# Kernel optimization log

Measured on AMD Instinct MI355X. Metric: run time of the kernel, lower is better.

## Reference

```python
import jax, jax.numpy as jnp
import numpy as np

EPS = 1e-5


def _tconv(x, W, b):
    # x: [M, Cin, S], W: [Cout, Cin, K] -> [M, Cout, S] (SAME padding)
    y = jax.lax.conv_general_dilated(x, W, window_strides=(1,), padding='SAME',
                                     dimension_numbers=('NCH', 'OIH', 'NCH'))
    return y + b[None, :, None]


def _bn(x, g, b, axes, pshape):
    # batch-statistics normalization (train-mode BN, deterministic)
    m = jnp.mean(x, axes, keepdims=True)
    v = jnp.var(x, axes, keepdims=True)
    return (x - m) * jax.lax.rsqrt(v + EPS) * g.reshape(pshape) + b.reshape(pshape)


def setup_inputs() -> dict:
    key = jax.random.key(0)
    ks = jax.random.split(key, 12)
    B, Cin, N, S = 4, 32, 1024, 32
    Cout, Csp, E, K = 64, 64, 16384, 3
    x = jax.random.normal(ks[0], (B, Cin, N, S), dtype=jnp.float32)
    edge_index = jax.random.randint(ks[1], (2, E), 0, N, dtype=jnp.int64)
    sc = 0.05
    return {
        'x': x,
        'edge_index': edge_index,
        'W1': jax.random.normal(ks[2], (Cout, Cin, K), dtype=jnp.float32) * sc,
        'b1': jnp.zeros((Cout,), jnp.float32),
        'g1': jnp.ones((Cout,), jnp.float32),
        'be1': jnp.zeros((Cout,), jnp.float32),
        'Wg': jax.random.normal(ks[3], (Cout, Csp), dtype=jnp.float32) * sc,
        'bg': jnp.zeros((Csp,), jnp.float32),
        'gs': jnp.ones((Csp,), jnp.float32),
        'bes': jnp.zeros((Csp,), jnp.float32),
        'W2': jax.random.normal(ks[4], (Cout, Csp, K), dtype=jnp.float32) * sc,
        'b2': jnp.zeros((Cout,), jnp.float32),
        'g2': jnp.ones((Cout,), jnp.float32),
        'be2': jnp.zeros((Cout,), jnp.float32),
        'Wres': jax.random.normal(ks[5], (Cout, Cin, 1), dtype=jnp.float32) * sc,
        'bres': jnp.zeros((Cout,), jnp.float32),
    }


def reference(x, edge_index, W1, b1, g1, be1, Wg, bg, gs, bes, W2, b2, g2, be2, Wres, bres):
    B, Cin, N, S = x.shape
    Cout = W1.shape[0]
    Csp = Wg.shape[1]

    # ---- temporal1: [B*N, Cin, S] -> [B*N, Cout, S] ----
    x1 = x.transpose(0, 2, 1, 3).reshape(B * N, Cin, S)
    h = jax.nn.relu(_bn(_tconv(x1, W1, b1), g1, be1, (0, 2), (1, -1, 1)))

    # ---- spatial GCN, all B*S timesteps in one pass ----
    h = h.reshape(B, N, Cout, S).transpose(0, 3, 1, 2)  # [B, S, N, Cout]
    hw = jnp.einsum('bsnc,cd->bsnd', h, Wg)             # [B, S, N, Csp]

    # self-loops + symmetric normalization (PyG GCNConv)
    loops = jnp.arange(N, dtype=edge_index.dtype)
    src = jnp.concatenate([edge_index[0], loops])
    dst = jnp.concatenate([edge_index[1], loops])
    deg = jax.ops.segment_sum(jnp.ones_like(src, dtype=hw.dtype), dst, num_segments=N)
    dinv = jnp.where(deg > 0, jax.lax.rsqrt(deg), 0.0)
    norm = (dinv[src] * dinv[dst])[None, None, :, None]  # [1,1,E+N,1]

    msg = hw[:, :, src, :] * norm                        # [B, S, E+N, Csp]
    agg = jnp.zeros_like(hw).at[:, :, dst, :].add(msg) + bg

    # per-timestep BatchNorm1d over the node dim (loop normalized each [N, Csp] slice)
    s = jax.nn.relu(_bn(agg, gs, bes, (2,), (1, 1, 1, -1)))  # dropout: eval mode

    # ---- temporal2: [B*N, Csp, S] -> [B*N, Cout, S] ----
    s = s.transpose(0, 2, 3, 1).reshape(B * N, Csp, S)   # [B,S,N,C] -> [B,N,C,S]
    h2 = jax.nn.relu(_bn(_tconv(s, W2, b2), g2, be2, (0, 2), (1, -1, 1)))
    h2 = h2.reshape(B, N, Cout, S)

    # ---- residual 1x1 conv ----
    res = _tconv(x1, Wres, bres).reshape(B, N, Cout, S)

    out = jax.nn.relu(h2 + res).transpose(0, 2, 1, 3)    # [B, Cout, N, S]
    return out
```

## Files before the change

kernel.cpp:

```cpp
#include <hip/hip_runtime.h>
#include <stdint.h>

#define B_    4
#define CIN   32
#define NN    1024
#define SS    32
#define COUT  64
#define CSP   64
#define EPSV  1e-5f

typedef __attribute__((ext_vector_type(8))) short bfrag;
typedef __attribute__((ext_vector_type(4))) float facc;

__device__ __forceinline__ uint32_t f2b_rne(float f) {
    uint32_t x = __float_as_uint(f);
    return (x + 0x7fffu + ((x >> 16) & 1u)) >> 16;
}
__device__ __forceinline__ float bfu(uint32_t v) { return __uint_as_float(v << 16); }
__device__ __forceinline__ float bfh(uint32_t v) { return __uint_as_float(v & 0xffff0000u); }

__global__ void pack_zero_kernel(const float* __restrict__ W1,
                                 const float* __restrict__ W2,
                                 const float* __restrict__ Wg,
                                 uint32_t* __restrict__ wpk1H, uint32_t* __restrict__ wpk1L,
                                 uint32_t* __restrict__ wpkH, uint32_t* __restrict__ wpkL,
                                 uint32_t* __restrict__ wgpH, uint32_t* __restrict__ wgpL,
                                 int* __restrict__ deg, int* __restrict__ cursor) {
    int blk = blockIdx.x, t = threadIdx.x;
    if (blk < 6) {
        int flat = blk * 256 + t;
        int lane = flat & 63, fi = flat >> 6;
        int kh = fi & 1, q = fi >> 1;
        int tap = q % 3, cc = q / 3;
        int ct = cc & 1, cb2 = cc >> 1;
        int cout = cb2 * 32 + ct * 16 + (lane & 15);
        int cbase = kh * 32 + (lane >> 4) * 8;
        const float* wp = W2 + ((size_t)cout * 64 + cbase) * 3 + tap;
        uint32_t h[8], l[8];
#pragma unroll
        for (int j = 0; j < 8; j++) {
            float w = wp[3 * j];
            uint32_t hb = f2b_rne(w);
            uint32_t lb = f2b_rne(w - bfu(hb));
            h[j] = hb; l[j] = lb;
        }
        uint4 H = {h[0] | (h[1] << 16), h[2] | (h[3] << 16),
                   h[4] | (h[5] << 16), h[6] | (h[7] << 16)};
        uint4 L = {l[0] | (l[1] << 16), l[2] | (l[3] << 16),
                   l[4] | (l[5] << 16), l[6] | (l[7] << 16)};
        ((uint4*)wpkH)[flat] = H;
        ((uint4*)wpkL)[flat] = L;
    } else if (blk < 9) {
        int flat = (blk - 6) * 256 + t;
        int lane = flat & 63, fi = flat >> 6;
        int tap = fi % 3, cc = fi / 3;
        int ct = cc & 1, cb2 = cc >> 1;
        int cout = cb2 * 32 + ct * 16 + (lane & 15);
        int k0 = (lane >> 4) * 8;
        const float* wp = W1 + (size_t)cout * 96 + k0 * 3 + tap;
        uint32_t h[8], l[8];
#pragma unroll
        for (int j = 0; j < 8; j++) {
            float w = wp[3 * j];
            uint32_t hb = f2b_rne(w);
            uint32_t lb = f2b_rne(w - bfu(hb));
            h[j] = hb; l[j] = lb;
        }
        uint4 H = {h[0] | (h[1] << 16), h[2] | (h[3] << 16),
                   h[4] | (h[5] << 16), h[6] | (h[7] << 16)};
        uint4 L = {l[0] | (l[1] << 16), l[2] | (l[3] << 16),
                   l[4] | (l[5] << 16), l[6] | (l[7] << 16)};
        ((uint4*)wpk1H)[flat] = H;
        ((uint4*)wpk1L)[flat] = L;
    } else if (blk < 11) {
        int flat = (blk - 9) * 256 + t;
        int lane = flat & 63, fi = flat >> 6;
        int kh = fi & 1, dt = fi >> 1;
        int d = dt * 16 + (lane & 15);
        int c0 = kh * 32 + (lane >> 4) * 8;
        const float* wp = Wg + (size_t)c0 * CSP + d;
        uint32_t h[8], l[8];
#pragma unroll
        for (int j = 0; j < 8; j++) {
            float w = wp[(size_t)j * CSP];
            uint32_t hb = f2b_rne(w);
            uint32_t lb = f2b_rne(w - bfu(hb));
            h[j] = hb; l[j] = lb;
        }
        uint4 H = {h[0] | (h[1] << 16), h[2] | (h[3] << 16),
                   h[4] | (h[5] << 16), h[6] | (h[7] << 16)};
        uint4 L = {l[0] | (l[1] << 16), l[2] | (l[3] << 16),
                   l[4] | (l[5] << 16), l[6] | (l[7] << 16)};
        ((uint4*)wgpH)[flat] = H;
        ((uint4*)wgpL)[flat] = L;
    } else {
        int4 z = {0, 0, 0, 0};
        ((int4*)deg)[t] = z;
        ((int4*)cursor)[t] = z;
    }
}

__global__ void deg_count_kernel(const int* __restrict__ ei, int E,
                                 int* __restrict__ deg) {
    __shared__ int snz;
    int t = threadIdx.x;
    if (t == 0) snz = 0;
    __syncthreads();
    if (t < 128 && ei[2 * t + 1] != 0) atomicOr(&snz, 1);
    __syncthreads();
    int i64 = (snz == 0) ? 1 : 0;
    int e = blockIdx.x * 256 + t;
    if (e < E) {
        int d = i64 ? ei[2 * (E + e)] : ei[E + e];
        atomicAdd(&deg[d], 1);
    }
}

__global__ __launch_bounds__(1024) void scan_kernel(
    const int* __restrict__ deg, int* __restrict__ row_ptr, float* __restrict__ dinv) {
    __shared__ int sb[NN];
    int t = threadIdx.x;
    int v = deg[t];
    sb[t] = v;
    __syncthreads();
    for (int off = 1; off < NN; off <<= 1) {
        int tmp = (t >= off) ? sb[t - off] : 0;
        __syncthreads();
        sb[t] += tmp;
        __syncthreads();
    }
    row_ptr[t] = sb[t] - v;
    if (t == NN - 1) row_ptr[NN] = sb[t];
    dinv[t] = rsqrtf((float)(v + 1));
}

__global__ void csr_fill_kernel(const int* __restrict__ ei, int E,
                                const int* __restrict__ row_ptr, int* __restrict__ cursor,
                                const float* __restrict__ dinv, int2* __restrict__ edata) {
    __shared__ int snz;
    int t = threadIdx.x;
    if (t == 0) snz = 0;
    __syncthreads();
    if (t < 128 && ei[2 * t + 1] != 0) atomicOr(&snz, 1);
    __syncthreads();
    int i64 = (snz == 0) ? 1 : 0;
    int e = blockIdx.x * 256 + t;
    if (e < E) {
        int s = i64 ? ei[2 * e] : ei[e];
        int d = i64 ? ei[2 * (E + e)] : ei[E + e];
        int pos = atomicAdd(&cursor[d], 1);
        edata[row_ptr[d] + pos] = make_int2(s, __float_as_int(dinv[s]));
    }
}

__global__ __launch_bounds__(256, 2) void conv1_mfma_kernel(
    const float* __restrict__ x, const uint32_t* __restrict__ wpk1H,
    const uint32_t* __restrict__ wpk1L, const float* __restrict__ b1,
    float* __restrict__ h_pre, float* __restrict__ psumC, float* __restrict__ pssC) {
    __shared__ __align__(16) char pool[18432];
    char* Phi = pool;
    char* Plo = pool + 8704;
    float* redS = (float*)(pool + 17408);
    float* redQ = (float*)(pool + 17920);
    int t = threadIdx.x;
    int grp = blockIdx.x;
    int b = grp >> 8, n0 = (grp & 255) * 4;
    int lane = t & 63, wv = t >> 6;
    int s0 = (wv >> 1) * 16, cb = (wv & 1) * 32;
    int l15 = lane & 15, lg = lane >> 4;

    if (t < 32) {
        int nl = t >> 3, rem = t & 7;
        int row = (rem >> 2) ? 33 : 0;
        int q = rem & 3;
        uint32_t off = (uint32_t)(nl * 2176 + row * 64 + q * 16);
        off ^= (uint32_t)((row & 7) << 4);
        *(uint4*)(Phi + off) = make_uint4(0u, 0u, 0u, 0u);
        *(uint4*)(Plo + off) = make_uint4(0u, 0u, 0u, 0u);
    }
#pragma unroll
    for (int it = 0; it < 2; it++) {
        int flat = it * 256 + t;
        int cinp = flat & 15;
        int nl = (flat >> 4) & 3;
        int s4 = (flat >> 6) * 4;
        const float* xp = x + (((size_t)b * CIN + 2 * cinp) * NN + n0 + nl) * SS + s4;
        float4 u0 = *(const float4*)xp;
        float4 u1 = *(const float4*)(xp + NN * SS);
        float va[4] = {u0.x, u0.y, u0.z, u0.w};
        float vb[4] = {u1.x, u1.y, u1.z, u1.w};
#pragma unroll
        for (int j = 0; j < 4; j++) {
            uint32_t ha = f2b_rne(va[j]), hb = f2b_rne(vb[j]);
            uint32_t la = f2b_rne(va[j] - bfu(ha)), lb = f2b_rne(vb[j] - bfu(hb));
            int row = s4 + j + 1;
            uint32_t off = (uint32_t)(nl * 2176 + row * 64 + cinp * 4);
            off ^= (uint32_t)((row & 7) << 4);
            *(uint32_t*)(Phi + off) = ha | (hb << 16);
            *(uint32_t*)(Plo + off) = la | (lb << 16);
        }
    }
    bfrag Wh[2][3], Wl[2][3];
    {
        const uint4* WH = (const uint4*)wpk1H;
        const uint4* WL = (const uint4*)wpk1L;
        int cb2 = wv & 1;
#pragma unroll
        for (int ct = 0; ct < 2; ct++)
#pragma unroll
            for (int tap = 0; tap < 3; tap++) {
                int fi = ((cb2 * 2 + ct) * 3 + tap) * 64 + lane;
                uint4 H = WH[fi];
                uint4 L = WL[fi];
                Wh[ct][tap] = *(const bfrag*)&H;
                Wl[ct][tap] = *(const bfrag*)&L;
            }
    }
    __syncthreads();

    float bb0 = b1[cb + l15], bb1 = b1[cb + 16 + l15];
    float sS0 = 0.f, sS1 = 0.f, sQ0 = 0.f, sQ1 = 0.f;
    for (int nl = 0; nl < 4; nl++) {
        facc acc0 = {0.f, 0.f, 0.f, 0.f};
        facc acc1 = {0.f, 0.f, 0.f, 0.f};
#pragma unroll
        for (int tap = 0; tap < 3; tap++) {
            int row = s0 + tap + l15;
            uint32_t off = (uint32_t)(nl * 2176 + row * 64 + (lg << 4));
            off ^= (uint32_t)((row & 7) << 4);
            bfrag ah = *(const bfrag*)(Phi + off);
            bfrag al = *(const bfrag*)(Plo + off);
            acc0 = __builtin_amdgcn_mfma_f32_16x16x32_bf16(ah, Wh[0][tap], acc0, 0, 0, 0);
            acc1 = __builtin_amdgcn_mfma_f32_16x16x32_bf16(ah, Wh[1][tap], acc1, 0, 0, 0);
            acc0 = __builtin_amdgcn_mfma_f32_16x16x32_bf16(al, Wh[0][tap], acc0, 0, 0, 0);
            acc1 = __builtin_amdgcn_mfma_f32_16x16x32_bf16(al, Wh[1][tap], acc1, 0, 0, 0);
            acc0 = __builtin_amdgcn_mfma_f32_16x16x32_bf16(ah, Wl[0][tap], acc0, 0, 0, 0);
            acc1 = __builtin_amdgcn_mfma_f32_16x16x32_bf16(ah, Wl[1][tap], acc1, 0, 0, 0);
        }
        int sx = s0 + (lg << 2);
        float* hp = h_pre + ((size_t)(b * NN + n0 + nl)) * (COUT * SS);
        {
            float y0 = acc0[0] + bb0, y1 = acc0[1] + bb0;
            float y2 = acc0[2] + bb0, y3 = acc0[3] + bb0;
            float4 o = {y0, y1, y2, y3};
            *(float4*)(hp + (cb + l15) * SS + sx) = o;
            sS0 += y0 + y1 + y2 + y3;
            sQ0 += y0 * y0 + y1 * y1 + y2 * y2 + y3 * y3;
        }
        {
            float y0 = acc1[0] + bb1, y1 = acc1[1] + bb1;
            float y2 = acc1[2] + bb1, y3 = acc1[3] + bb1;
            float4 o = {y0, y1, y2, y3};
            *(float4*)(hp + (cb + 16 + l15) * SS + sx) = o;
            sS1 += y0 + y1 + y2 + y3;
            sQ1 += y0 * y0 + y1 * y1 + y2 * y2 + y3 * y3;
        }
    }
    sS0 += __shfl_down(sS0, 16); sS0 += __shfl_down(sS0, 32);
    sS1 += __shfl_down(sS1, 16); sS1 += __shfl_down(sS1, 32);
    sQ0 += __shfl_down(sQ0, 16); sQ0 += __shfl_down(sQ0, 32);
    sQ1 += __shfl_down(sQ1, 16); sQ1 += __shfl_down(sQ1, 32);
    if (lane < 16) {
        redS[wv * 32 + lane] = sS0;      redQ[wv * 32 + lane] = sQ0;
        redS[wv * 32 + 16 + lane] = sS1; redQ[wv * 32 + 16 + lane] = sQ1;
    }
    __syncthreads();
    if (t < 64) {
        int wA = t >> 5, slot = t & 31;
        float S = redS[wA * 32 + slot] + redS[(wA + 2) * 32 + slot];
        float Q = redQ[wA * 32 + slot] + redQ[(wA + 2) * 32 + slot];
        psumC[(size_t)t * 1024 + grp] = S;
        pssC[(size_t)t * 1024 + grp] = Q;
    }
}

__global__ void bn_reduce_kernel(const float* __restrict__ psum, const float* __restrict__ pss,
                                 const float* __restrict__ g, const float* __restrict__ be,
                                 float* __restrict__ scale, float* __restrict__ shift,
                                 float invM, int stride, int nslots) {
    int c = blockIdx.x, t = threadIdx.x;
    const float* ps = psum + c * stride;
    const float* pq = pss + c * stride;
    float s = 0.f, q = 0.f;
    for (int i = t; i < nslots; i += 256) { s += ps[i]; q += pq[i]; }
#pragma unroll
    for (int o = 32; o > 0; o >>= 1) { s += __shfl_down(s, o); q += __shfl_down(q, o); }
    __shared__ float ws_[4], wq_[4];
    if ((t & 63) == 0) { ws_[t >> 6] = s; wq_[t >> 6] = q; }
    __syncthreads();
    if (t == 0) {
        float S = ws_[0] + ws_[1] + ws_[2] + ws_[3];
        float Q = wq_[0] + wq_[1] + wq_[2] + wq_[3];
        float m = S * invM, v = Q * invM - m * m;
        float sc = g[c] * rsqrtf(v + EPSV);
        scale[c] = sc;
        shift[c] = be[c] - m * sc;
    }
}

__global__ __launch_bounds__(256, 2) void bn1_gemm_mfma_kernel(
    const float* __restrict__ h_pre, const float* __restrict__ scale1,
    const float* __restrict__ shift1, const uint32_t* __restrict__ wgpH,
    const uint32_t* __restrict__ wgpL, ushort* __restrict__ hw) {
    __shared__ __align__(16) char pool[32768];
    char* Xhi = pool;
    char* Xlo = pool + 16384;
    int t = threadIdx.x;
    int grp = blockIdx.x;
    int b = grp >> 8, n0 = (grp & 255) * 4;
    int lane = t & 63, wv = t >> 6;
    int l15 = lane & 15, lg = lane >> 4;

#pragma unroll
    for (int it = 0; it < 4; it++) {
        int flat = it * 256 + t;
        int sq = flat & 7;
        int nl = (flat >> 3) & 3;
        int cp = flat >> 5;
        int c = 2 * cp;
        int s4 = sq * 4;
        const float* p = h_pre + (((size_t)(b * NN + n0 + nl)) * COUT + c) * SS + s4;
        float4 u0 = *(const float4*)p;
        float4 u1 = *(const float4*)(p + SS);
        float scA = scale1[c], shA = shift1[c];
        float scB = scale1[c + 1], shB = shift1[c + 1];
        float va[4] = {fmaxf(u0.x * scA + shA, 0.f), fmaxf(u0.y * scA + shA, 0.f),
                       fmaxf(u0.z * scA + shA, 0.f), fmaxf(u0.w * scA + shA, 0.f)};
        float vb[4] = {fmaxf(u1.x * scB + shB, 0.f), fmaxf(u1.y * scB + shB, 0.f),
                       fmaxf(u1.z * scB + shB, 0.f), fmaxf(u1.w * scB + shB, 0.f)};
#pragma unroll
        for (int j = 0; j < 4; j++) {
            uint32_t ha = f2b_rne(va[j]), hb = f2b_rne(vb[j]);
            uint32_t la = f2b_rne(va[j] - bfu(ha)), lb = f2b_rne(vb[j] - bfu(hb));
            int row = nl * 32 + s4 + j;
            uint32_t off = (uint32_t)(row * 128 + 4 * cp);
            off ^= (uint32_t)((row & 7) << 4);
            *(uint32_t*)(Xhi + off) = ha | (hb << 16);
            *(uint32_t*)(Xlo + off) = la | (lb << 16);
        }
    }
    bfrag WgH[4][2], WgL[4][2];
    {
        const uint4* WH = (const uint4*)wgpH;
        const uint4* WL = (const uint4*)wgpL;
#pragma unroll
        for (int dt = 0; dt < 4; dt++)
#pragma unroll
            for (int kh = 0; kh < 2; kh++) {
                int fi = (dt * 2 + kh) * 64 + lane;
                uint4 H = WH[fi];
                uint4 L = WL[fi];
                WgH[dt][kh] = *(const bfrag*)&H;
                WgL[dt][kh] = *(const bfrag*)&L;
            }
    }
    __syncthreads();

    int n = n0 + wv;
#pragma unroll
    for (int rt = 0; rt < 2; rt++) {
        facc a0 = {0.f, 0.f, 0.f, 0.f};
        facc a1 = {0.f, 0.f, 0.f, 0.f};
        facc a2 = {0.f, 0.f, 0.f, 0.f};
        facc a3 = {0.f, 0.f, 0.f, 0.f};
#pragma unroll
        for (int kh = 0; kh < 2; kh++) {
            int row = wv * 32 + rt * 16 + l15;
            uint32_t off = (uint32_t)(row * 128 + kh * 64 + (lg << 4));
            off ^= (uint32_t)((row & 7) << 4);
            bfrag xh = *(const bfrag*)(Xhi + off);
            bfrag xl = *(const bfrag*)(Xlo + off);
            a0 = __builtin_amdgcn_mfma_f32_16x16x32_bf16(WgH[0][kh], xh, a0, 0, 0, 0);
            a1 = __builtin_amdgcn_mfma_f32_16x16x32_bf16(WgH[1][kh], xh, a1, 0, 0, 0);
            a2 = __builtin_amdgcn_mfma_f32_16x16x32_bf16(WgH[2][kh], xh, a2, 0, 0, 0);
            a3 = __builtin_amdgcn_mfma_f32_16x16x32_bf16(WgH[3][kh], xh, a3, 0, 0, 0);
            a0 = __builtin_amdgcn_mfma_f32_16x16x32_bf16(WgL[0][kh], xh, a0, 0, 0, 0);
            a1 = __builtin_amdgcn_mfma_f32_16x16x32_bf16(WgL[1][kh], xh, a1, 0, 0, 0);
            a2 = __builtin_amdgcn_mfma_f32_16x16x32_bf16(WgL[2][kh], xh, a2, 0, 0, 0);
            a3 = __builtin_amdgcn_mfma_f32_16x16x32_bf16(WgL[3][kh], xh, a3, 0, 0, 0);
            a0 = __builtin_amdgcn_mfma_f32_16x16x32_bf16(WgH[0][kh], xl, a0, 0, 0, 0);
            a1 = __builtin_amdgcn_mfma_f32_16x16x32_bf16(WgH[1][kh], xl, a1, 0, 0, 0);
            a2 = __builtin_amdgcn_mfma_f32_16x16x32_bf16(WgH[2][kh], xl, a2, 0, 0, 0);
            a3 = __builtin_amdgcn_mfma_f32_16x16x32_bf16(WgH[3][kh], xl, a3, 0, 0, 0);
        }
        int s = rt * 16 + l15;
        ushort* op = hw + (((size_t)(b * NN + n)) * SS + s) * CSP;
        {
            uint32_t p0 = f2b_rne(a0[0]) | (f2b_rne(a0[1]) << 16);
            uint32_t p1 = f2b_rne(a0[2]) | (f2b_rne(a0[3]) << 16);
            *(uint2*)(op + 0 * 16 + lg * 4) = make_uint2(p0, p1);
        }
        {
            uint32_t p0 = f2b_rne(a1[0]) | (f2b_rne(a1[1]) << 16);
            uint32_t p1 = f2b_rne(a1[2]) | (f2b_rne(a1[3]) << 16);
            *(uint2*)(op + 1 * 16 + lg * 4) = make_uint2(p0, p1);
        }
        {
            uint32_t p0 = f2b_rne(a2[0]) | (f2b_rne(a2[1]) << 16);
            uint32_t p1 = f2b_rne(a2[2]) | (f2b_rne(a2[3]) << 16);
            *(uint2*)(op + 2 * 16 + lg * 4) = make_uint2(p0, p1);
        }
        {
            uint32_t p0 = f2b_rne(a3[0]) | (f2b_rne(a3[1]) << 16);
            uint32_t p1 = f2b_rne(a3[2]) | (f2b_rne(a3[3]) << 16);
            *(uint2*)(op + 3 * 16 + lg * 4) = make_uint2(p0, p1);
        }
    }
}

__global__ __launch_bounds__(256, 4) void gcn_kernel(
    const ushort* __restrict__ hw, const int* __restrict__ row_ptr,
    const int2* __restrict__ edata, const float* __restrict__ dinv,
    const float* __restrict__ bg, float* __restrict__ agg,
    float* __restrict__ psum2, float* __restrict__ pss2) {
    int t = threadIdx.x;
    int blk = blockIdx.x;
    int xcd = blk & 7, jj = blk >> 3;
    int b = xcd >> 1;
    int grp = (xcd & 1) + 2 * jj;
    int n0 = grp * 4;
    int off = t * 8;
    const ushort* hwb = hw + (size_t)b * NN * 2048;
    float bgv[8];
    int c0 = off & 63;
#pragma unroll
    for (int j = 0; j < 8; j++) bgv[j] = bg[c0 + j];
    float sS[8], sQ[8];
#pragma unroll
    for (int j = 0; j < 8; j++) { sS[j] = 0.f; sQ[j] = 0.f; }
    for (int g = 0; g < 4; g++) {
        int n = n0 + g;
        int r0 = row_ptr[n], r1 = row_ptr[n + 1];
        float dn = dinv[n];
        float acc[8];
        {
            uint4 u = *(const uint4*)(hwb + (size_t)n * 2048 + off);
            acc[0] = dn * bfu(u.x); acc[1] = dn * bfh(u.x);
            acc[2] = dn * bfu(u.y); acc[3] = dn * bfh(u.y);
            acc[4] = dn * bfu(u.z); acc[5] = dn * bfh(u.z);
            acc[6] = dn * bfu(u.w); acc[7] = dn * bfh(u.w);
        }
        int r = r0;
        for (; r + 4 <= r1; r += 4) {
            int2 e0 = edata[r], e1 = edata[r + 1];
            int2 e2 = edata[r + 2], e3 = edata[r + 3];
            uint4 u0 = *(const uint4*)(hwb + (size_t)e0.x * 2048 + off);
            uint4 u1 = *(const uint4*)(hwb + (size_t)e1.x * 2048 + off);
            uint4 u2 = *(const uint4*)(hwb + (size_t)e2.x * 2048 + off);
            uint4 u3 = *(const uint4*)(hwb + (size_t)e3.x * 2048 + off);
            float w0 = __int_as_float(e0.y), w1 = __int_as_float(e1.y);
            float w2 = __int_as_float(e2.y), w3 = __int_as_float(e3.y);
            acc[0] += w0 * bfu(u0.x) + w1 * bfu(u1.x);
            acc[1] += w0 * bfh(u0.x) + w1 * bfh(u1.x);
            acc[2] += w0 * bfu(u0.y) + w1 * bfu(u1.y);
            acc[3] += w0 * bfh(u0.y) + w1 * bfh(u1.y);
            acc[4] += w0 * bfu(u0.z) + w1 * bfu(u1.z);
            acc[5] += w0 * bfh(u0.z) + w1 * bfh(u1.z);
            acc[6] += w0 * bfu(u0.w) + w1 * bfu(u1.w);
            acc[7] += w0 * bfh(u0.w) + w1 * bfh(u1.w);
            acc[0] += w2 * bfu(u2.x) + w3 * bfu(u3.x);
            acc[1] += w2 * bfh(u2.x) + w3 * bfh(u3.x);
            acc[2] += w2 * bfu(u2.y) + w3 * bfu(u3.y);
            acc[3] += w2 * bfh(u2.y) + w3 * bfh(u3.y);
            acc[4] += w2 * bfu(u2.z) + w3 * bfu(u3.z);
            acc[5] += w2 * bfh(u2.z) + w3 * bfh(u3.z);
            acc[6] += w2 * bfu(u2.w) + w3 * bfu(u3.w);
            acc[7] += w2 * bfh(u2.w) + w3 * bfh(u3.w);
        }
        for (; r < r1; r++) {
            int2 e = edata[r];
            uint4 u = *(const uint4*)(hwb + (size_t)e.x * 2048 + off);
            float w = __int_as_float(e.y);
            acc[0] += w * bfu(u.x); acc[1] += w * bfh(u.x);
            acc[2] += w * bfu(u.y); acc[3] += w * bfh(u.y);
            acc[4] += w * bfu(u.z); acc[5] += w * bfh(u.z);
            acc[6] += w * bfu(u.w); acc[7] += w * bfh(u.w);
        }
        float o[8];
#pragma unroll
        for (int j = 0; j < 8; j++) {
            o[j] = dn * acc[j] + bgv[j];
            sS[j] += o[j]; sQ[j] += o[j] * o[j];
        }
        float* ar = agg + ((size_t)(b * NN + n)) * 2048 + off;
        float4 o0 = {o[0], o[1], o[2], o[3]}, o1 = {o[4], o[5], o[6], o[7]};
        *(float4*)ar = o0; *(float4*)(ar + 4) = o1;
    }
    float* ps = psum2 + ((size_t)(b * 256 + grp)) * 2048 + off;
    float* pq = pss2 + ((size_t)(b * 256 + grp)) * 2048 + off;
    float4 s0v = {sS[0], sS[1], sS[2], sS[3]}, s1v = {sS[4], sS[5], sS[6], sS[7]};
    float4 q0v = {sQ[0], sQ[1], sQ[2], sQ[3]}, q1v = {sQ[4], sQ[5], sQ[6], sQ[7]};
    *(float4*)ps = s0v; *(float4*)(ps + 4) = s1v;
    *(float4*)pq = q0v; *(float4*)(pq + 4) = q1v;
}

__global__ __launch_bounds__(256) void bn2_reduce_kernel(
    const float* __restrict__ psum2, const float* __restrict__ pss2,
    const float* __restrict__ gs, const float* __restrict__ bes,
    float* __restrict__ scale2, float* __restrict__ shift2) {
    __shared__ float redS[4][32], redQ[4][32];
    int t = threadIdx.x;
    int slot = blockIdx.x * 32 + (t & 31);
    int b = slot >> 11, rem = slot & 2047;
    int chunk = t >> 5;
    const float* ps = psum2 + ((size_t)(b * 256 + chunk * 32)) * 2048 + rem;
    const float* pq = pss2 + ((size_t)(b * 256 + chunk * 32)) * 2048 + rem;
    float S = 0.f, Q = 0.f;
#pragma unroll 8
    for (int i = 0; i < 32; i++) {
        S += ps[(size_t)i * 2048];
        Q += pq[(size_t)i * 2048];
    }
    S += __shfl_down(S, 32);
    Q += __shfl_down(Q, 32);
    int w = t >> 6;
    if ((t & 63) < 32) { redS[w][t & 31] = S; redQ[w][t & 31] = Q; }
    __syncthreads();
    if (t < 32) {
        float Sf = redS[0][t] + redS[1][t] + redS[2][t] + redS[3][t];
        float Qf = redQ[0][t] + redQ[1][t] + redQ[2][t] + redQ[3][t];
        int slot0 = blockIdx.x * 32 + t;
        int d = slot0 & 63;
        float m = Sf * (1.f / NN);
        float v = Qf * (1.f / NN) - m * m;
        float sc = gs[d] * rsqrtf(v + EPSV);
        scale2[slot0] = sc;
        shift2[slot0] = bes[d] - m * sc;
    }
}

__global__ __launch_bounds__(256, 2) void conv2_mfma_kernel(
    const float* __restrict__ agg, const float* __restrict__ scale2,
    const float* __restrict__ shift2, const uint32_t* __restrict__ wpkH,
    const uint32_t* __restrict__ wpkL,
    const float* __restrict__ b2, float* __restrict__ h2_pre,
    float* __restrict__ psumC, float* __restrict__ pssC) {
    __shared__ __align__(16) char pool[35840];
    char* Phi = pool;
    char* Plo = pool + 17408;
    float* redS = (float*)(pool + 34816);
    float* redQ = (float*)(pool + 35328);
    int t = threadIdx.x;
    int grp = blockIdx.x;
    int b = grp >> 8, n0 = (grp & 255) * 4;
    int lane = t & 63, wv = t >> 6;
    int s0 = (wv >> 1) * 16, cb = (wv & 1) * 32;
    int l15 = lane & 15, lg = lane >> 4;

    if (t < 128) {
        int nl = t >> 5, rem = t & 31;
        int tr = (rem >> 4) ? 33 : 0;
        int j = rem & 15;
        uint32_t off = (uint32_t)(nl * 4352 + tr * 128 + 8 * j);
        off ^= (uint32_t)((tr & 7) << 4);
        *(uint2*)(Phi + off) = make_uint2(0u, 0u);
        *(uint2*)(Plo + off) = make_uint2(0u, 0u);
    }
#pragma unroll
    for (int i = 0; i < 8; i++) {
        int flat4 = i * 256 + t;
        int c0 = 4 * (flat4 & 15);
        int s = (flat4 >> 4) & 31;
        int nl = flat4 >> 9;
        const float* p = agg + ((size_t)((b * NN + n0 + nl) * 32 + s)) * 64 + c0;
        float4 u = *(const float4*)p;
        int bsi = (b * 32 + s) * 64 + c0;
        float4 sc = *(const float4*)(scale2 + bsi);
        float4 sh = *(const float4*)(shift2 + bsi);
        float v0 = fmaxf(u.x * sc.x + sh.x, 0.f);
        float v1 = fmaxf(u.y * sc.y + sh.y, 0.f);
        float v2 = fmaxf(u.z * sc.z + sh.z, 0.f);
        float v3 = fmaxf(u.w * sc.w + sh.w, 0.f);
        uint32_t h0 = f2b_rne(v0), h1 = f2b_rne(v1), h2 = f2b_rne(v2), h3 = f2b_rne(v3);
        uint32_t l0 = f2b_rne(v0 - bfu(h0)), l1 = f2b_rne(v1 - bfu(h1));
        uint32_t l2 = f2b_rne(v2 - bfu(h2)), l3 = f2b_rne(v3 - bfu(h3));
        int tr = s + 1;
        uint32_t off = (uint32_t)(nl * 4352 + tr * 128 + 2 * c0);
        off ^= (uint32_t)((tr & 7) << 4);
        *(uint2*)(Phi + off) = make_uint2(h0 | (h1 << 16), h2 | (h3 << 16));
        *(uint2*)(Plo + off) = make_uint2(l0 | (l1 << 16), l2 | (l3 << 16));
    }

    bfrag Wh[2][3][2], Wl[2][3][2];
    {
        const uint4* WH = (const uint4*)wpkH;
        const uint4* WL = (const uint4*)wpkL;
        int cb2 = wv & 1;
#pragma unroll
        for (int ct = 0; ct < 2; ct++)
#pragma unroll
            for (int tap = 0; tap < 3; tap++)
#pragma unroll
                for (int kh = 0; kh < 2; kh++) {
                    int fi = ((((cb2 * 2 + ct) * 3 + tap) * 2) + kh) * 64 + lane;
                    uint4 H = WH[fi];
                    uint4 L = WL[fi];
                    Wh[ct][tap][kh] = *(const bfrag*)&H;
                    Wl[ct][tap][kh] = *(const bfrag*)&L;
                }
    }
    __syncthreads();

    float bb0 = b2[cb + l15], bb1 = b2[cb + 16 + l15];
    float sS0 = 0.f, sS1 = 0.f, sQ0 = 0.f, sQ1 = 0.f;
    for (int nl = 0; nl < 4; nl++) {
        facc acc0 = {0.f, 0.f, 0.f, 0.f};
        facc acc1 = {0.f, 0.f, 0.f, 0.f};
#pragma unroll
        for (int tap = 0; tap < 3; tap++) {
#pragma unroll
            for (int kh = 0; kh < 2; kh++) {
                int row = s0 + tap + l15;
                uint32_t off = (uint32_t)(nl * 4352 + row * 128 + kh * 64 + (lg << 4));
                off ^= (uint32_t)((row & 7) << 4);
                bfrag ah = *(const bfrag*)(Phi + off);
                bfrag al = *(const bfrag*)(Plo + off);
                acc0 = __builtin_amdgcn_mfma_f32_16x16x32_bf16(ah, Wh[0][tap][kh], acc0, 0, 0, 0);
                acc1 = __builtin_amdgcn_mfma_f32_16x16x32_bf16(ah, Wh[1][tap][kh], acc1, 0, 0, 0);
                acc0 = __builtin_amdgcn_mfma_f32_16x16x32_bf16(al, Wh[0][tap][kh], acc0, 0, 0, 0);
                acc1 = __builtin_amdgcn_mfma_f32_16x16x32_bf16(al, Wh[1][tap][kh], acc1, 0, 0, 0);
                acc0 = __builtin_amdgcn_mfma_f32_16x16x32_bf16(ah, Wl[0][tap][kh], acc0, 0, 0, 0);
                acc1 = __builtin_amdgcn_mfma_f32_16x16x32_bf16(ah, Wl[1][tap][kh], acc1, 0, 0, 0);
            }
        }
        int sx = s0 + (lg << 2);
        float* hp = h2_pre + ((size_t)(b * NN + n0 + nl)) * (COUT * SS);
        {
            float y0 = acc0[0] + bb0, y1 = acc0[1] + bb0;
            float y2 = acc0[2] + bb0, y3 = acc0[3] + bb0;
            float4 o = {y0, y1, y2, y3};
            *(float4*)(hp + (cb + l15) * SS + sx) = o;
            sS0 += y0 + y1 + y2 + y3;
            sQ0 += y0 * y0 + y1 * y1 + y2 * y2 + y3 * y3;
        }
        {
            float y0 = acc1[0] + bb1, y1 = acc1[1] + bb1;
            float y2 = acc1[2] + bb1, y3 = acc1[3] + bb1;
            float4 o = {y0, y1, y2, y3};
            *(float4*)(hp + (cb + 16 + l15) * SS + sx) = o;
            sS1 += y0 + y1 + y2 + y3;
            sQ1 += y0 * y0 + y1 * y1 + y2 * y2 + y3 * y3;
        }
    }
    sS0 += __shfl_down(sS0, 16); sS0 += __shfl_down(sS0, 32);
    sS1 += __shfl_down(sS1, 16); sS1 += __shfl_down(sS1, 32);
    sQ0 += __shfl_down(sQ0, 16); sQ0 += __shfl_down(sQ0, 32);
    sQ1 += __shfl_down(sQ1, 16); sQ1 += __shfl_down(sQ1, 32);
    if (lane < 16) {
        redS[wv * 32 + lane] = sS0;      redQ[wv * 32 + lane] = sQ0;
        redS[wv * 32 + 16 + lane] = sS1; redQ[wv * 32 + 16 + lane] = sQ1;
    }
    __syncthreads();
    if (t < 64) {
        int wA = t >> 5, slot = t & 31;
        float S = redS[wA * 32 + slot] + redS[(wA + 2) * 32 + slot];
        float Q = redQ[wA * 32 + slot] + redQ[(wA + 2) * 32 + slot];
        psumC[(size_t)t * 1024 + grp] = S;
        pssC[(size_t)t * 1024 + grp] = Q;
    }
}

__global__ __launch_bounds__(256) void final_kernel(
    const float* __restrict__ x, const float* __restrict__ Wres,
    const float* __restrict__ bres, const float* __restrict__ h2_pre,
    const float* __restrict__ scale3, const float* __restrict__ shift3,
    float* __restrict__ out) {
    __shared__ __align__(16) float xs[CIN][36];
    __shared__ float wrl[COUT * 33];
    int t = threadIdx.x;
    int bn = blockIdx.x;
    int b = bn >> 10, n = bn & (NN - 1);
    {
        int sst = t & 31, cinb = t >> 5;
#pragma unroll
        for (int i = 0; i < 4; i++) {
            int cin = cinb + 8 * i;
            xs[cin][sst] = x[(((size_t)b * CIN + cin) * NN + n) * SS + sst];
        }
    }
#pragma unroll
    for (int i = 0; i < 2; i++) {
        int lin = (i * 256 + t) * 4;
        int cw = lin >> 5, c0 = lin & 31;
        float4 v = *(const float4*)(Wres + lin);
        float* dst = &wrl[cw * 33 + c0];
        dst[0] = v.x; dst[1] = v.y; dst[2] = v.z; dst[3] = v.w;
    }
    __syncthreads();
    int cout = t >> 2, s0 = (t & 3) * 8;
    float res[8];
    float bb = bres[cout];
#pragma unroll
    for (int j = 0; j < 8; j++) res[j] = bb;
    const float* wrow = &wrl[cout * 33];
#pragma unroll 4
    for (int cin = 0; cin < CIN; cin++) {
        float w = wrow[cin];
        float4 xa = *(const float4*)&xs[cin][s0];
        float4 xb = *(const float4*)&xs[cin][s0 + 4];
        res[0] += xa.x * w; res[1] += xa.y * w; res[2] += xa.z * w; res[3] += xa.w * w;
        res[4] += xb.x * w; res[5] += xb.y * w; res[6] += xb.z * w; res[7] += xb.w * w;
    }
    const float* hp = h2_pre + (size_t)bn * COUT * SS + cout * SS + s0;
    float4 h0 = *(const float4*)hp, h1 = *(const float4*)(hp + 4);
    float h2[8] = {h0.x, h0.y, h0.z, h0.w, h1.x, h1.y, h1.z, h1.w};
    float sc = scale3[cout], sh = shift3[cout];
    float o[8];
#pragma unroll
    for (int j = 0; j < 8; j++) {
        float hv = fmaxf(sc * h2[j] + sh, 0.f);
        o[j] = fmaxf(hv + res[j], 0.f);
    }
    float* op = out + (((size_t)b * COUT + cout) * NN + n) * SS + s0;
    float4 o0 = {o[0], o[1], o[2], o[3]}, o1 = {o[4], o[5], o[6], o[7]};
    *(float4*)op = o0; *(float4*)(op + 4) = o1;
}

extern "C" void kernel_launch(void* const* d_in, const int* in_sizes, int n_in,
                              void* d_out, int out_size, void* d_ws, size_t ws_size,
                              hipStream_t stream) {
    const float* x    = (const float*)d_in[0];
    const int*   ei   = (const int*)  d_in[1];
    const float* W1   = (const float*)d_in[2];
    const float* b1   = (const float*)d_in[3];
    const float* g1   = (const float*)d_in[4];
    const float* be1  = (const float*)d_in[5];
    const float* Wg   = (const float*)d_in[6];
    const float* bg   = (const float*)d_in[7];
    const float* gs   = (const float*)d_in[8];
    const float* bes  = (const float*)d_in[9];
    const float* W2   = (const float*)d_in[10];
    const float* b2   = (const float*)d_in[11];
    const float* g2   = (const float*)d_in[12];
    const float* be2  = (const float*)d_in[13];
    const float* Wres = (const float*)d_in[14];
    const float* bres = (const float*)d_in[15];
    float* out = (float*)d_out;
    int E = in_sizes[1] / 2;

    char* ws = (char*)d_ws;
    int*   deg    = (int*)  (ws + 0);
    int*   cursor = (int*)  (ws + 4096);
    uint32_t* wpkH = (uint32_t*)(ws + 8192);
    uint32_t* wpkL = (uint32_t*)(ws + 32768);
    int*   row_ptr= (int*)  (ws + 73728);
    float* dinv   = (float*)(ws + 78080);
    float* scale1 = (float*)(ws + 82176);
    float* shift1 = (float*)(ws + 82432);
    float* scale3 = (float*)(ws + 82688);
    float* shift3 = (float*)(ws + 82944);
    float* scale2 = (float*)(ws + 83200);
    float* shift2 = (float*)(ws + 115968);
    int2*  edata  = (int2*) (ws + 410880);
    char*  bigA   = ws + 542720;
    ushort* hwB   = (ushort*)bigA;
    float* h2p    = (float*)bigA;
    float* psumC  = (float*)(ws + 34097152);
    float* pssC   = (float*)(ws + 34359296);
    uint32_t* wpk1H = (uint32_t*)(ws + 34621440);
    uint32_t* wpk1L = (uint32_t*)(ws + 34633728);
    uint32_t* wgpH  = (uint32_t*)(ws + 34646016);
    uint32_t* wgpL  = (uint32_t*)(ws + 34654208);
    float* psum2  = (float*)(ws + 35651584);
    float* pss2   = (float*)(ws + 52428800);
    float* h_pre  = out;
    float* agg    = out;

    pack_zero_kernel<<<12, 256, 0, stream>>>(W1, W2, Wg, wpk1H, wpk1L,
                                             wpkH, wpkL, wgpH, wgpL, deg, cursor);
    int egrid = (E + 255) / 256;
    deg_count_kernel<<<egrid, 256, 0, stream>>>(ei, E, deg);
    scan_kernel<<<1, NN, 0, stream>>>(deg, row_ptr, dinv);
    csr_fill_kernel<<<egrid, 256, 0, stream>>>(ei, E, row_ptr, cursor, dinv, edata);

    conv1_mfma_kernel<<<1024, 256, 0, stream>>>(x, wpk1H, wpk1L, b1, h_pre, psumC, pssC);
    bn_reduce_kernel<<<64, 256, 0, stream>>>(psumC, pssC, g1, be1, scale1, shift1,
                                             1.f / (B_ * NN * SS), 1024, 1024);
    bn1_gemm_mfma_kernel<<<1024, 256, 0, stream>>>(h_pre, scale1, shift1, wgpH, wgpL, hwB);
    gcn_kernel<<<1024, 256, 0, stream>>>(hwB, row_ptr, edata, dinv, bg, agg, psum2, pss2);
    bn2_reduce_kernel<<<256, 256, 0, stream>>>(psum2, pss2, gs, bes, scale2, shift2);
    conv2_mfma_kernel<<<1024, 256, 0, stream>>>(agg, scale2, shift2, wpkH, wpkL,
                                                b2, h2p, psumC, pssC);
    bn_reduce_kernel<<<64, 256, 0, stream>>>(psumC, pssC, g2, be2, scale3, shift3,
                                             1.f / (B_ * NN * SS), 1024, 1024);
    final_kernel<<<B_ * NN, 256, 0, stream>>>(x, Wres, bres, h2p, scale3, shift3, out);
}
```

Baseline: 205.7 us.

## Fuse graph preprocessing kernels into one cooperative launch with grid syncs

Merges the weight-pack/zero, degree count, prefix scan and CSR fill kernels into a single cooperative kernel separated by grid-wide syncs. The scan now runs in one 256-thread block with four elements per thread. This removes three kernel launches and their inter-kernel gaps, at the cost of grid-sync overhead and a cooperative-launch grid of 76 blocks.

```diff
diff --git a/kernel.cpp b/kernel.cpp
--- a/kernel.cpp
+++ b/kernel.cpp
@@ -1,5 +1,8 @@
 #include <hip/hip_runtime.h>
+#include <hip/hip_cooperative_groups.h>
 #include <stdint.h>
+
+namespace cg = cooperative_groups;
 
 #define B_    4
 #define CIN   32
@@ -19,14 +22,22 @@
 __device__ __forceinline__ float bfu(uint32_t v) { return __uint_as_float(v << 16); }
 __device__ __forceinline__ float bfh(uint32_t v) { return __uint_as_float(v & 0xffff0000u); }
 
-__global__ void pack_zero_kernel(const float* __restrict__ W1,
-                                 const float* __restrict__ W2,
-                                 const float* __restrict__ Wg,
-                                 uint32_t* __restrict__ wpk1H, uint32_t* __restrict__ wpk1L,
-                                 uint32_t* __restrict__ wpkH, uint32_t* __restrict__ wpkL,
-                                 uint32_t* __restrict__ wgpH, uint32_t* __restrict__ wgpL,
-                                 int* __restrict__ deg, int* __restrict__ cursor) {
+__global__ void graph_prep_kernel(
+    const int* __restrict__ ei, int E, int egrid,
+    const float* __restrict__ W1, const float* __restrict__ W2,
+    const float* __restrict__ Wg,
+    uint32_t* __restrict__ wpk1H, uint32_t* __restrict__ wpk1L,
+    uint32_t* __restrict__ wpkH, uint32_t* __restrict__ wpkL,
+    uint32_t* __restrict__ wgpH, uint32_t* __restrict__ wgpL,
+    int* __restrict__ deg, int* __restrict__ cursor,
+    int* __restrict__ row_ptr, float* __restrict__ dinv,
+    int2* __restrict__ edata) {
+    cg::grid_group grid = cg::this_grid();
+    __shared__ int sb[NN];
+    __shared__ int ts[256];
+    __shared__ int snz;
     int blk = blockIdx.x, t = threadIdx.x;
+
     if (blk < 6) {
         int flat = blk * 256 + t;
         int lane = flat & 63, fi = flat >> 6;
@@ -93,64 +104,67 @@
                    l[4] | (l[5] << 16), l[6] | (l[7] << 16)};
         ((uint4*)wgpH)[flat] = H;
         ((uint4*)wgpL)[flat] = L;
-    } else {
+    } else if (blk == 11) {
         int4 z = {0, 0, 0, 0};
         ((int4*)deg)[t] = z;
         ((int4*)cursor)[t] = z;
     }
-}
-
-__global__ void deg_count_kernel(const int* __restrict__ ei, int E,
-                                 int* __restrict__ deg) {
-    __shared__ int snz;
-    int t = threadIdx.x;
-    if (t == 0) snz = 0;
-    __syncthreads();
-    if (t < 128 && ei[2 * t + 1] != 0) atomicOr(&snz, 1);
-    __syncthreads();
-    int i64 = (snz == 0) ? 1 : 0;
-    int e = blockIdx.x * 256 + t;
-    if (e < E) {
-        int d = i64 ? ei[2 * (E + e)] : ei[E + e];
-        atomicAdd(&deg[d], 1);
-    }
-}
-
-__global__ __launch_bounds__(1024) void scan_kernel(
-    const int* __restrict__ deg, int* __restrict__ row_ptr, float* __restrict__ dinv) {
-    __shared__ int sb[NN];
-    int t = threadIdx.x;
-    int v = deg[t];
-    sb[t] = v;
-    __syncthreads();
-    for (int off = 1; off < NN; off <<= 1) {
-        int tmp = (t >= off) ? sb[t - off] : 0;
+    grid.sync();
+
+    if (blk >= 12) {
+        if (t == 0) snz = 0;
         __syncthreads();
-        sb[t] += tmp;
+        if (t < 128 && ei[2 * t + 1] != 0) atomicOr(&snz, 1);
         __syncthreads();
-    }
-    row_ptr[t] = sb[t] - v;
-    if (t == NN - 1) row_ptr[NN] = sb[t];
-    dinv[t] = rsqrtf((float)(v + 1));
-}
-
-__global__ void csr_fill_kernel(const int* __restrict__ ei, int E,
-                                const int* __restrict__ row_ptr, int* __restrict__ cursor,
-                                const float* __restrict__ dinv, int2* __restrict__ edata) {
-    __shared__ int snz;
-    int t = threadIdx.x;
-    if (t == 0) snz = 0;
-    __syncthreads();
-    if (t < 128 && ei[2 * t + 1] != 0) atomicOr(&snz, 1);
-    __syncthreads();
-    int i64 = (snz == 0) ? 1 : 0;
-    int e = blockIdx.x * 256 + t;
-    if (e < E) {
-        int s = i64 ? ei[2 * e] : ei[e];
-        int d = i64 ? ei[2 * (E + e)] : ei[E + e];
-        int pos = atomicAdd(&cursor[d], 1);
-        edata[row_ptr[d] + pos] = make_int2(s, __float_as_int(dinv[s]));
-    }
+        int i64 = (snz == 0) ? 1 : 0;
+        int e = (blk - 12) * 256 + t;
+        if (e < E) {
+            int d = i64 ? ei[2 * (E + e)] : ei[E + e];
+            atomicAdd(&deg[d], 1);
+        }
+    }
+    grid.sync();
+
+    if (blk == 0) {
+        int base = t * 4;
+        int a0 = deg[base], a1 = deg[base + 1], a2 = deg[base + 2], a3 = deg[base + 3];
+        int p1 = a0, p2 = a0 + a1, p3 = a0 + a1 + a2, tot = p3 + a3;
+        ts[t] = tot;
+        __syncthreads();
+        for (int off = 1; off < 256; off <<= 1) {
+            int tmp = (t >= off) ? ts[t - off] : 0;
+            __syncthreads();
+            ts[t] += tmp;
+            __syncthreads();
+        }
+        int excl = (t == 0) ? 0 : ts[t - 1];
+        row_ptr[base]     = excl;
+        row_ptr[base + 1] = excl + p1;
+        row_ptr[base + 2] = excl + p2;
+        row_ptr[base + 3] = excl + p3;
+        if (t == 255) row_ptr[NN] = ts[255];
+        dinv[base]     = rsqrtf((float)(a0 + 1));
+        dinv[base + 1] = rsqrtf((float)(a1 + 1));
+        dinv[base + 2] = rsqrtf((float)(a2 + 1));
+        dinv[base + 3] = rsqrtf((float)(a3 + 1));
+    }
+    grid.sync();
+
+    if (blk >= 12) {
+        if (t == 0) snz = 0;
+        __syncthreads();
+        if (t < 128 && ei[2 * t + 1] != 0) atomicOr(&snz, 1);
+        __syncthreads();
+        int i64 = (snz == 0) ? 1 : 0;
+        int e = (blk - 12) * 256 + t;
+        if (e < E) {
+            int s = i64 ? ei[2 * e] : ei[e];
+            int d = i64 ? ei[2 * (E + e)] : ei[E + e];
+            int pos = atomicAdd(&cursor[d], 1);
+            edata[row_ptr[d] + pos] = make_int2(s, __float_as_int(dinv[s]));
+        }
+    }
+    (void)sb;
 }
 
 __global__ __launch_bounds__(256, 2) void conv1_mfma_kernel(
@@ -766,12 +780,19 @@
     float* h_pre  = out;
     float* agg    = out;
 
-    pack_zero_kernel<<<12, 256, 0, stream>>>(W1, W2, Wg, wpk1H, wpk1L,
-                                             wpkH, wpkL, wgpH, wgpL, deg, cursor);
     int egrid = (E + 255) / 256;
-    deg_count_kernel<<<egrid, 256, 0, stream>>>(ei, E, deg);
-    scan_kernel<<<1, NN, 0, stream>>>(deg, row_ptr, dinv);
-    csr_fill_kernel<<<egrid, 256, 0, stream>>>(ei, E, row_ptr, cursor, dinv, edata);
+    {
+        void* args[] = {
+            (void*)&ei, (void*)&E, (void*)&egrid,
+            (void*)&W1, (void*)&W2, (void*)&Wg,
+            (void*)&wpk1H, (void*)&wpk1L, (void*)&wpkH, (void*)&wpkL,
+            (void*)&wgpH, (void*)&wgpL,
+            (void*)&deg, (void*)&cursor, (void*)&row_ptr, (void*)&dinv,
+            (void*)&edata,
+        };
+        hipLaunchCooperativeKernel(reinterpret_cast<void*>(graph_prep_kernel),
+                                   dim3(12 + egrid), dim3(256), args, 0, stream);
+    }
 
     conv1_mfma_kernel<<<1024, 256, 0, stream>>>(x, wpk1H, wpk1L, b1, h_pre, psumC, pssC);
     bn_reduce_kernel<<<64, 256, 0, stream>>>(psumC, pssC, g1, be1, scale1, shift1,
```

After: 258.9 us. +25.9%, slower.
